# Performance work log

Measured on AMD Instinct MI355X. Metric: run time of the kernel, lower is better.

The kernel has to match this reference:

```python
import jax, jax.numpy as jnp
import numpy as np

EMB = 512
HEADS = 8
WINDOW = 128


def setup_inputs() -> dict:
    key = jax.random.key(0)
    ks = jax.random.split(key, 9)
    s = 1.0 / np.sqrt(EMB)
    x = jax.random.normal(ks[0], (2, 4096, EMB), dtype=jnp.float32)
    mk = lambda k: jax.random.uniform(k, (EMB, EMB), jnp.float32, -s, s)
    mb = lambda k: jax.random.uniform(k, (EMB,), jnp.float32, -s, s)
    return {
        "x": x,
        "Wq": mk(ks[1]), "bq": mb(ks[2]),
        "Wk": mk(ks[3]), "bk": mb(ks[4]),
        "Wv": mk(ks[5]), "bv": mb(ks[6]),
        "Wo": mk(ks[7]), "bo": mb(ks[8]),
    }


def _split_heads(y, b, n):
    # [b, n, emb] -> [b, h, n, d]
    return y.reshape(b, n, HEADS, EMB // HEADS).transpose(0, 2, 1, 3)


def reference(x, Wq, bq, Wk, bk, Wv, bv, Wo, bo):
    b, n, _ = x.shape
    q = _split_heads(x @ Wq.T + bq, b, n)
    k = _split_heads(x @ Wk.T + bk, b, n)
    v = _split_heads(x @ Wv.T + bv, b, n)
    energy = jnp.einsum('bhqd,bhkd->bhqk', q, k)  # [b,h,n,n]
    idx = jnp.arange(n)
    # banded mask: disallowed where |i - j| > window (matches torch loop)
    disallow = jnp.abs(idx[:, None] - idx[None, :]) > WINDOW
    fmin = jnp.float32(np.finfo(np.float32).min)
    energy = jnp.where(disallow[None, None], fmin, energy)
    att = jax.nn.softmax(energy / jnp.float32(np.sqrt(EMB)), axis=-1)
    out = jnp.einsum('bhql,bhld->bhqd', att, v)
    out = out.transpose(0, 2, 1, 3).reshape(b, n, EMB)
    return out @ Wo.T + bo
```

## Files before the change

kernel.cpp:

```cpp
#include <hip/hip_runtime.h>

#define EMB 512
#define HEADS 8
#define HD 64
#define NSEQ 4096
#define BATCH 2
#define WINDOW 128

typedef unsigned short u16;
typedef __attribute__((ext_vector_type(8))) short bf16x8;
typedef __attribute__((ext_vector_type(4))) float f32x4;

#define XS 4194304u
#define WS 262144u
#define BS 512u

__device__ __forceinline__ float bf2f(u16 u) {
    union { unsigned int i; float f; } x;
    x.i = ((unsigned int)u) << 16;
    return x.f;
}

__device__ __forceinline__ u16 f2bf(float f) {
    union { float f; unsigned int i; } x;
    x.f = f;
    unsigned int i = x.i;
    unsigned int lsb = (i >> 16) & 1u;
    i += 0x7fffu + lsb;
    return (u16)(i >> 16);
}

struct raw8 { uint4 lo, hi; };

__device__ __forceinline__ raw8 loadraw8(const void* base, size_t off, int isbf) {
    raw8 r;
    if (isbf) {
        r.lo = *(const uint4*)((const u16*)base + off);
    } else {
        const float* f = (const float*)base + off;
        r.lo = *(const uint4*)f;
        r.hi = *(const uint4*)(f + 4);
    }
    return r;
}

__device__ __forceinline__ uint4 cvt8(const raw8& r, int isbf) {
    if (isbf) return r.lo;
    const float* a = (const float*)&r.lo;
    const float* b = (const float*)&r.hi;
    uint4 o;
    o.x = (unsigned)f2bf(a[0]) | ((unsigned)f2bf(a[1]) << 16);
    o.y = (unsigned)f2bf(a[2]) | ((unsigned)f2bf(a[3]) << 16);
    o.z = (unsigned)f2bf(b[0]) | ((unsigned)f2bf(b[1]) << 16);
    o.w = (unsigned)f2bf(b[2]) | ((unsigned)f2bf(b[3]) << 16);
    return o;
}

__device__ __forceinline__ int probe_bf16(const void* p) {
    const int lane = threadIdx.x & 63;
    u16 w = ((const u16*)p)[lane * 2];
    int e = (w >> 7) & 0xff;
    bool sane = (w == 0) || (e >= 100 && e <= 140);
    unsigned long long m = __ballot(sane);
    return __popcll(m) >= 48;
}

__global__ __launch_bounds__(256)
void prepass(const void* __restrict__ x,
             const void* __restrict__ Wq, const void* __restrict__ bq,
             const void* __restrict__ Wk, const void* __restrict__ bk,
             const void* __restrict__ Wv, const void* __restrict__ bv,
             const void* __restrict__ Wo, const void* __restrict__ bo,
             u16* __restrict__ xb, u16* __restrict__ wb, u16* __restrict__ bb,
             int* __restrict__ flags)
{
    const int fx  = probe_bf16(x);
    const int fwq = probe_bf16(Wq), fbq = probe_bf16(bq);
    const int fwk = probe_bf16(Wk), fbk = probe_bf16(bk);
    const int fwv = probe_bf16(Wv), fbv = probe_bf16(bv);
    const int fwo = probe_bf16(Wo), fbo = probe_bf16(bo);
    if (blockIdx.x == 0 && threadIdx.x == 0) flags[0] = fx;

    size_t idx = ((size_t)blockIdx.x * 256 + threadIdx.x) * 8;
    const size_t T_X = XS, T_W = XS + 4 * (size_t)WS, T_ALL = T_W + 4 * (size_t)BS;
    if (idx >= T_ALL) return;

    const void* src; int fl; u16* dst; size_t off;
    if (idx < T_X) {
        src = x; fl = fx; dst = xb; off = idx;
    } else if (idx < T_W) {
        size_t w = idx - T_X;
        int wi = (int)(w / WS); off = w % WS;
        src = (wi == 0) ? Wq : (wi == 1) ? Wk : (wi == 2) ? Wv : Wo;
        fl  = (wi == 0) ? fwq : (wi == 1) ? fwk : (wi == 2) ? fwv : fwo;
        dst = wb + (size_t)wi * WS;
    } else {
        size_t b = idx - T_W;
        int bi = (int)(b / BS); off = b % BS;
        src = (bi == 0) ? bq : (bi == 1) ? bk : (bi == 2) ? bv : bo;
        fl  = (bi == 0) ? fbq : (bi == 1) ? fbk : (bi == 2) ? fbv : fbo;
        dst = bb + (size_t)bi * BS;
    }
    *(uint4*)(dst + off) = cvt8(loadraw8(src, off, fl), fl);
}

__global__ __launch_bounds__(512)
void qkv_gemm(const u16* __restrict__ X, const u16* __restrict__ Wall,
              const u16* __restrict__ ball,
              u16* __restrict__ qo, u16* __restrict__ ko, u16* __restrict__ vo)
{
    __shared__ __align__(16) u16 As2[2][128 * 32];
    __shared__ __align__(16) u16 Bs2[2][128 * 32];

    const int tid  = threadIdx.x;
    const int wave = tid >> 6;
    const int lane = tid & 63;
    const int quad = lane >> 4;
    const int l16  = lane & 15;
    const int wm = wave >> 2, wn = wave & 3;

    const int m0 = blockIdx.x * 128;
    const int by = blockIdx.y;
    const int wsel = by >> 2;
    const int n0 = (by & 3) * 128;

    const u16* W  = Wall + (size_t)wsel * WS;
    const u16* bi = ball + (size_t)wsel * BS;
    const float oscale = (wsel == 0) ? 0.04419417382415922f : 1.0f;

    const u16* PA = (wsel == 2) ? W : X;
    const u16* PB = (wsel == 2) ? X : W;
    const int abase = (wsel == 2) ? n0 : m0;
    const int bbase = (wsel == 2) ? m0 : n0;

    f32x4 acc[4][2];
#pragma unroll
    for (int i = 0; i < 4; ++i)
#pragma unroll
        for (int j = 0; j < 2; ++j)
            acc[i][j] = (f32x4){0.f, 0.f, 0.f, 0.f};

    const int r1 = tid >> 2, k1 = (tid & 3) * 8;

    const u16* pa = PA + (size_t)(abase + r1) * EMB + k1;
    const u16* pb = PB + (size_t)(bbase + r1) * EMB + k1;

    uint4 a1 = *(const uint4*)pa;
    uint4 b1 = *(const uint4*)pb;
    *(uint4*)&As2[0][tid * 8] = a1;
    *(uint4*)&Bs2[0][tid * 8] = b1;
    a1 = *(const uint4*)(pa + 32);
    b1 = *(const uint4*)(pb + 32);
    __syncthreads();

    for (int kt = 0; kt < 16; ++kt) {
        const int cur = kt & 1;

        bf16x8 af[4], bfr[2];
#pragma unroll
        for (int i = 0; i < 4; ++i)
            af[i] = *(const bf16x8*)&As2[cur][(wm * 64 + i * 16 + l16) * 32 + quad * 8];
#pragma unroll
        for (int j = 0; j < 2; ++j)
            bfr[j] = *(const bf16x8*)&Bs2[cur][(wn * 32 + j * 16 + l16) * 32 + quad * 8];

        if (kt < 15) {
            *(uint4*)&As2[cur ^ 1][tid * 8] = a1;
            *(uint4*)&Bs2[cur ^ 1][tid * 8] = b1;
        }
        if (kt < 14) {
            const int kk0 = (kt + 2) * 32;
            a1 = *(const uint4*)(pa + kk0);
            b1 = *(const uint4*)(pb + kk0);
        }

#pragma unroll
        for (int i = 0; i < 4; ++i)
#pragma unroll
            for (int j = 0; j < 2; ++j)
                acc[i][j] = __builtin_amdgcn_mfma_f32_16x16x32_bf16(af[i], bfr[j], acc[i][j], 0, 0, 0);

        if (kt < 15) __syncthreads();
    }

    if (wsel != 2) {
#pragma unroll
        for (int j = 0; j < 2; ++j) {
            const int col = n0 + wn * 32 + j * 16 + l16;
            const float bv_ = bf2f(bi[col]);
            const int h = col >> 6, d = col & 63;
            u16* out = (wsel == 0) ? qo : ko;
#pragma unroll
            for (int i = 0; i < 4; ++i) {
#pragma unroll
                for (int r = 0; r < 4; ++r) {
                    const int row = m0 + wm * 64 + i * 16 + quad * 4 + r;
                    const int b = row >> 12, n = row & 4095;
                    out[(((size_t)(b * HEADS + h) * NSEQ) + n) * HD + d] =
                        f2bf((acc[i][j][r] + bv_) * oscale);
                }
            }
        }
    } else {
#pragma unroll
        for (int i = 0; i < 4; ++i) {
#pragma unroll
            for (int r = 0; r < 4; ++r) {
                const int dglob = n0 + wm * 64 + i * 16 + quad * 4 + r;
                const float bv_ = bf2f(bi[dglob]);
                const int h = dglob >> 6, dd = dglob & 63;
#pragma unroll
                for (int j = 0; j < 2; ++j) {
                    const int ncol = m0 + wn * 32 + j * 16 + l16;
                    const int b = ncol >> 12, n = ncol & 4095;
                    vo[((size_t)(b * HEADS + h) * HD + dd) * NSEQ + n] =
                        f2bf(acc[i][j][r] + bv_);
                }
            }
        }
    }
}

#define KP 72
#define VP 72
__global__ __launch_bounds__(256)
void attn_mfma(const u16* __restrict__ q, const u16* __restrict__ k,
               const u16* __restrict__ vt, u16* __restrict__ ao)
{
    __shared__ __align__(16) u16 Ks2[2][64 * KP];
    __shared__ __align__(16) u16 Vt2[2][64 * VP];
    __shared__ __align__(16) u16 Vones[16 * VP];
    __shared__ __align__(16) u16 Pb[4][16 * KP];

    const int tid  = threadIdx.x;
    const int wave = tid >> 6;
    const int lane = tid & 63;
    const int quad = lane >> 4;
    const int l16  = lane & 15;

    int wg = blockIdx.y * 64 + blockIdx.x;
    wg = (wg & 7) * 128 + (wg >> 3);
    const int bh = wg >> 6;
    const int q0 = (wg & 63) * 64;

    const int qw = q0 + wave * 16;
    const size_t base = (size_t)bh * NSEQ * HD;
    const bool interior = (q0 >= 128) && (q0 <= NSEQ - 192);

    if (tid < VP) {
        Vones[tid] = (u16)0x3f80;
#pragma unroll
        for (int rr = 1; rr < 16; ++rr) Vones[rr * VP + tid] = 0;
    }

    bf16x8 qa0 = *(const bf16x8*)(q + base + (size_t)(qw + l16) * HD + quad * 8);
    bf16x8 qa1 = *(const bf16x8*)(q + base + (size_t)(qw + l16) * HD + 32 + quad * 8);

    f32x4 O[4], O4;
#pragma unroll
    for (int t = 0; t < 4; ++t) O[t] = (f32x4){0.f, 0.f, 0.f, 0.f};
    O4 = (f32x4){0.f, 0.f, 0.f, 0.f};

    const int key_s[2] = { tid >> 3, (tid + 256) >> 3 };
    const int ch8      = (tid & 7) * 8;

    const int pacol = (quad * 8) ^ ((l16 >> 2) << 4);

    uint4 pkv[2], pvv[2];
#pragma unroll
    for (int s = 0; s < 2; ++s) {
        int kg = q0 - 128 + key_s[s];
        kg = (kg < 0) ? 0 : (kg > NSEQ - 1 ? NSEQ - 1 : kg);
        pkv[s] = *(const uint4*)(k + base + (size_t)kg * HD + ch8);
        int kc = q0 - 128 + ch8;
        kc = (kc < 0) ? 0 : (kc > NSEQ - 8 ? NSEQ - 8 : kc);
        pvv[s] = *(const uint4*)(vt + base + (size_t)key_s[s] * NSEQ + kc);
    }
#pragma unroll
    for (int s = 0; s < 2; ++s) {
        *(uint4*)&Ks2[0][key_s[s] * KP + ch8] = pkv[s];
        *(uint4*)&Vt2[0][key_s[s] * VP + ch8] = pvv[s];
    }
#pragma unroll
    for (int s = 0; s < 2; ++s) {
        int kg = q0 - 64 + key_s[s];
        kg = (kg < 0) ? 0 : (kg > NSEQ - 1 ? NSEQ - 1 : kg);
        pkv[s] = *(const uint4*)(k + base + (size_t)kg * HD + ch8);
        int kc = q0 - 64 + ch8;
        kc = (kc < 0) ? 0 : (kc > NSEQ - 8 ? NSEQ - 8 : kc);
        pvv[s] = *(const uint4*)(vt + base + (size_t)key_s[s] * NSEQ + kc);
    }
    __syncthreads();

    for (int c = 0; c < 5; ++c) {
        const int cur = c & 1;
        const int kbase = q0 - 128 + c * 64;

        if (c < 4) {
#pragma unroll
            for (int s = 0; s < 2; ++s) {
                *(uint4*)&Ks2[cur ^ 1][key_s[s] * KP + ch8] = pkv[s];
                *(uint4*)&Vt2[cur ^ 1][key_s[s] * VP + ch8] = pvv[s];
            }
        }
        if (c < 3) {
            const int nb = kbase + 128;
#pragma unroll
            for (int s = 0; s < 2; ++s) {
                int kg = nb + key_s[s];
                kg = (kg < 0) ? 0 : (kg > NSEQ - 1 ? NSEQ - 1 : kg);
                pkv[s] = *(const uint4*)(k + base + (size_t)kg * HD + ch8);
                int kc = nb + ch8;
                kc = (kc < 0) ? 0 : (kc > NSEQ - 8 ? NSEQ - 8 : kc);
                pvv[s] = *(const uint4*)(vt + base + (size_t)key_s[s] * NSEQ + kc);
            }
        }

        const int gdk = kbase - qw;
        const bool act = (gdk <= 143) && (gdk >= -191) &&
                         (kbase > -64) && (kbase < NSEQ);
        if (act) {
            f32x4 sv[4];
#pragma unroll
            for (int t = 0; t < 4; ++t) {
                const int dk = gdk + t * 16;
                if (dk >= -143 && dk <= 143) {
                    bf16x8 b0 = *(const bf16x8*)&Ks2[cur][(t * 16 + l16) * KP + quad * 8];
                    bf16x8 b1 = *(const bf16x8*)&Ks2[cur][(t * 16 + l16) * KP + 32 + quad * 8];
                    f32x4 sacc = (f32x4){0.f, 0.f, 0.f, 0.f};
                    sacc = __builtin_amdgcn_mfma_f32_16x16x32_bf16(qa0, b0, sacc, 0, 0, 0);
                    sacc = __builtin_amdgcn_mfma_f32_16x16x32_bf16(qa1, b1, sacc, 0, 0, 0);
                    if (!interior || dk < -113 || dk > 113) {
                        const int jg = kbase + t * 16 + l16;
                        const bool jok = ((unsigned)jg) < (unsigned)NSEQ;
#pragma unroll
                        for (int r = 0; r < 4; ++r) {
                            const int iq = qw + quad * 4 + r;
                            const bool band = ((unsigned)(iq - jg + WINDOW)) <= (unsigned)(2 * WINDOW);
                            if (!(jok && band)) sacc[r] = -1e30f;
                        }
                    }
                    sv[t] = sacc;
                } else {
                    sv[t] = (f32x4){-1e30f, -1e30f, -1e30f, -1e30f};
                }
            }

#pragma unroll
            for (int t = 0; t < 4; ++t) {
                const int tc = (t ^ quad) * 16 + l16;
#pragma unroll
                for (int r = 0; r < 4; ++r) {
                    const float pv = __expf(fminf(sv[t][r], 40.f));
                    Pb[wave][(quad * 4 + r) * KP + tc] = f2bf(pv);
                }
            }

#pragma unroll
            for (int ks2 = 0; ks2 < 2; ++ks2) {
                bf16x8 pa = *(const bf16x8*)&Pb[wave][l16 * KP + (pacol ^ (ks2 * 32))];
#pragma unroll
                for (int t = 0; t < 4; ++t) {
                    bf16x8 vb = *(const bf16x8*)&Vt2[cur][(t * 16 + l16) * VP + ks2 * 32 + quad * 8];
                    O[t] = __builtin_amdgcn_mfma_f32_16x16x32_bf16(pa, vb, O[t], 0, 0, 0);
                }
                bf16x8 vb4 = *(const bf16x8*)&Vones[l16 * VP + ks2 * 32 + quad * 8];
                O4 = __builtin_amdgcn_mfma_f32_16x16x32_bf16(pa, vb4, O4, 0, 0, 0);
            }
        }

        if (c < 4) __syncthreads();
    }

    const int bb = bh >> 3, hh = bh & 7;
    float rl[4];
#pragma unroll
    for (int r = 0; r < 4; ++r) {
        const float ls = __shfl(O4[r], lane & 48, 64);
        rl[r] = 1.f / ls;
    }
#pragma unroll
    for (int t = 0; t < 4; ++t)
#pragma unroll
        for (int r = 0; r < 4; ++r) {
            const int iq = qw + quad * 4 + r;
            ao[((size_t)(bb * NSEQ + iq)) * EMB + hh * HD + t * 16 + l16] =
                f2bf(O[t][r] * rl[r]);
        }
}

__global__ __launch_bounds__(512)
void out_gemm(const u16* __restrict__ A, const u16* __restrict__ W,
              const u16* __restrict__ bias, void* __restrict__ out,
              const int* __restrict__ flags)
{
    __shared__ __align__(16) u16 As2[2][128 * 32];
    __shared__ __align__(16) u16 Bs2[2][128 * 32];

    const int tid  = threadIdx.x;
    const int wave = tid >> 6;
    const int lane = tid & 63;
    const int quad = lane >> 4;
    const int l16  = lane & 15;
    const int wm = wave >> 2, wn = wave & 3;

    const int m0 = blockIdx.x * 128;
    const int n0 = blockIdx.y * 128;
    const int fo = flags[0];

    f32x4 acc[4][2];
#pragma unroll
    for (int i = 0; i < 4; ++i)
#pragma unroll
        for (int j = 0; j < 2; ++j)
            acc[i][j] = (f32x4){0.f, 0.f, 0.f, 0.f};

    const int r1 = tid >> 2, k1 = (tid & 3) * 8;

    uint4 a1 = *(const uint4*)(A + (size_t)(m0 + r1) * EMB + k1);
    uint4 b1 = *(const uint4*)(W + (size_t)(n0 + r1) * EMB + k1);
    *(uint4*)&As2[0][tid * 8] = a1;
    *(uint4*)&Bs2[0][tid * 8] = b1;
    a1 = *(const uint4*)(A + (size_t)(m0 + r1) * EMB + 32 + k1);
    b1 = *(const uint4*)(W + (size_t)(n0 + r1) * EMB + 32 + k1);
    __syncthreads();

    for (int kt = 0; kt < 16; ++kt) {
        const int cur = kt & 1;

        bf16x8 af[4], bfr[2];
#pragma unroll
        for (int i = 0; i < 4; ++i)
            af[i] = *(const bf16x8*)&As2[cur][(wm * 64 + i * 16 + l16) * 32 + quad * 8];
#pragma unroll
        for (int j = 0; j < 2; ++j)
            bfr[j] = *(const bf16x8*)&Bs2[cur][(wn * 32 + j * 16 + l16) * 32 + quad * 8];

        if (kt < 15) {
            *(uint4*)&As2[cur ^ 1][tid * 8] = a1;
            *(uint4*)&Bs2[cur ^ 1][tid * 8] = b1;
        }
        if (kt < 14) {
            const int kk0 = (kt + 2) * 32;
            a1 = *(const uint4*)(A + (size_t)(m0 + r1) * EMB + kk0 + k1);
            b1 = *(const uint4*)(W + (size_t)(n0 + r1) * EMB + kk0 + k1);
        }

#pragma unroll
        for (int i = 0; i < 4; ++i)
#pragma unroll
            for (int j = 0; j < 2; ++j)
                acc[i][j] = __builtin_amdgcn_mfma_f32_16x16x32_bf16(af[i], bfr[j], acc[i][j], 0, 0, 0);

        if (kt < 15) __syncthreads();
    }

#pragma unroll
    for (int j = 0; j < 2; ++j) {
        const int col = n0 + wn * 32 + j * 16 + l16;
        const float bv_ = bf2f(bias[col]);
#pragma unroll
        for (int i = 0; i < 4; ++i) {
#pragma unroll
            for (int r = 0; r < 4; ++r) {
                const int row = m0 + wm * 64 + i * 16 + quad * 4 + r;
                const float val = acc[i][j][r] + bv_;
                const size_t idx = (size_t)row * EMB + col;
                if (fo) ((u16*)out)[idx] = f2bf(val);
                else    ((float*)out)[idx] = val;
            }
        }
    }
}

extern "C" void kernel_launch(void* const* d_in, const int* in_sizes, int n_in,
                              void* d_out, int out_size, void* d_ws, size_t ws_size,
                              hipStream_t stream)
{
    const size_t HSZ  = (size_t)BATCH * HEADS * NSEQ * HD;
    char* base = (char*)d_ws;
    int* flags = (int*)base;
    const size_t off = 256;

    u16* xb = (u16*)(base + off);
    u16* wb = xb + XS;
    u16* bb = wb + 4 * (size_t)WS;
    u16* kk = bb + 4 * (size_t)BS;
    u16* vv = kk + HSZ;
    u16* ao = vv + HSZ;
    u16* qq = ao + HSZ;

    const size_t need_t1 = off + 2 * (XS + 4 * (size_t)WS + 4 * (size_t)BS + 4 * HSZ);
    if (ws_size < need_t1) {
        qq = (u16*)d_out;
    }

    prepass<<<dim3(2561), 256, 0, stream>>>(d_in[0], d_in[1], d_in[2], d_in[3],
                                            d_in[4], d_in[5], d_in[6], d_in[7],
                                            d_in[8], xb, wb, bb, flags);
    qkv_gemm<<<dim3(64, 12), 512, 0, stream>>>(xb, wb, bb, qq, kk, vv);
    attn_mfma<<<dim3(64, 16), 256, 0, stream>>>(qq, kk, vv, ao);
    out_gemm<<<dim3(64, 4), 512, 0, stream>>>(ao, wb + 3 * (size_t)WS, bb + 3 * (size_t)BS,
                                              d_out, flags);
}
```

Measured before the change: 146.0 us.

## Probe only the source tensor in prepass; use 1024 threads in out_gemm

```diff
diff --git a/kernel.cpp b/kernel.cpp
--- a/kernel.cpp
+++ b/kernel.cpp
@@ -74,33 +74,26 @@
              u16* __restrict__ xb, u16* __restrict__ wb, u16* __restrict__ bb,
              int* __restrict__ flags)
 {
-    const int fx  = probe_bf16(x);
-    const int fwq = probe_bf16(Wq), fbq = probe_bf16(bq);
-    const int fwk = probe_bf16(Wk), fbk = probe_bf16(bk);
-    const int fwv = probe_bf16(Wv), fbv = probe_bf16(bv);
-    const int fwo = probe_bf16(Wo), fbo = probe_bf16(bo);
-    if (blockIdx.x == 0 && threadIdx.x == 0) flags[0] = fx;
-
     size_t idx = ((size_t)blockIdx.x * 256 + threadIdx.x) * 8;
     const size_t T_X = XS, T_W = XS + 4 * (size_t)WS, T_ALL = T_W + 4 * (size_t)BS;
     if (idx >= T_ALL) return;
 
-    const void* src; int fl; u16* dst; size_t off;
+    const void* src; u16* dst; size_t off;
     if (idx < T_X) {
-        src = x; fl = fx; dst = xb; off = idx;
+        src = x; dst = xb; off = idx;
     } else if (idx < T_W) {
         size_t w = idx - T_X;
         int wi = (int)(w / WS); off = w % WS;
         src = (wi == 0) ? Wq : (wi == 1) ? Wk : (wi == 2) ? Wv : Wo;
-        fl  = (wi == 0) ? fwq : (wi == 1) ? fwk : (wi == 2) ? fwv : fwo;
         dst = wb + (size_t)wi * WS;
     } else {
         size_t b = idx - T_W;
         int bi = (int)(b / BS); off = b % BS;
         src = (bi == 0) ? bq : (bi == 1) ? bk : (bi == 2) ? bv : bo;
-        fl  = (bi == 0) ? fbq : (bi == 1) ? fbk : (bi == 2) ? fbv : fbo;
         dst = bb + (size_t)bi * BS;
     }
+    const int fl = probe_bf16(src);
+    if (idx == 0) flags[0] = fl;
     *(uint4*)(dst + off) = cvt8(loadraw8(src, off, fl), fl);
 }
 
@@ -389,7 +382,7 @@
         }
 }
 
-__global__ __launch_bounds__(512)
+__global__ __launch_bounds__(1024)
 void out_gemm(const u16* __restrict__ A, const u16* __restrict__ W,
               const u16* __restrict__ bias, void* __restrict__ out,
               const int* __restrict__ flags)
@@ -408,46 +401,47 @@
     const int n0 = blockIdx.y * 128;
     const int fo = flags[0];
 
-    f32x4 acc[4][2];
-#pragma unroll
-    for (int i = 0; i < 4; ++i)
+    f32x4 acc[2][2];
+#pragma unroll
+    for (int i = 0; i < 2; ++i)
 #pragma unroll
         for (int j = 0; j < 2; ++j)
             acc[i][j] = (f32x4){0.f, 0.f, 0.f, 0.f};
 
-    const int r1 = tid >> 2, k1 = (tid & 3) * 8;
-
-    uint4 a1 = *(const uint4*)(A + (size_t)(m0 + r1) * EMB + k1);
-    uint4 b1 = *(const uint4*)(W + (size_t)(n0 + r1) * EMB + k1);
-    *(uint4*)&As2[0][tid * 8] = a1;
-    *(uint4*)&Bs2[0][tid * 8] = b1;
-    a1 = *(const uint4*)(A + (size_t)(m0 + r1) * EMB + 32 + k1);
-    b1 = *(const uint4*)(W + (size_t)(n0 + r1) * EMB + 32 + k1);
+    const int half = tid >> 9;
+    const int t2   = tid & 511;
+    const int r1 = t2 >> 2, k1 = (t2 & 3) * 8;
+
+    const u16* P = half ? (W + (size_t)(n0 + r1) * EMB + k1)
+                        : (A + (size_t)(m0 + r1) * EMB + k1);
+
+    uint4 v1 = *(const uint4*)P;
+    if (half) *(uint4*)&Bs2[0][t2 * 8] = v1;
+    else      *(uint4*)&As2[0][t2 * 8] = v1;
+    v1 = *(const uint4*)(P + 32);
     __syncthreads();
 
     for (int kt = 0; kt < 16; ++kt) {
         const int cur = kt & 1;
 
-        bf16x8 af[4], bfr[2];
-#pragma unroll
-        for (int i = 0; i < 4; ++i)
-            af[i] = *(const bf16x8*)&As2[cur][(wm * 64 + i * 16 + l16) * 32 + quad * 8];
+        bf16x8 af[2], bfr[2];
+#pragma unroll
+        for (int i = 0; i < 2; ++i)
+            af[i] = *(const bf16x8*)&As2[cur][(wm * 32 + i * 16 + l16) * 32 + quad * 8];
 #pragma unroll
         for (int j = 0; j < 2; ++j)
             bfr[j] = *(const bf16x8*)&Bs2[cur][(wn * 32 + j * 16 + l16) * 32 + quad * 8];
 
         if (kt < 15) {
-            *(uint4*)&As2[cur ^ 1][tid * 8] = a1;
-            *(uint4*)&Bs2[cur ^ 1][tid * 8] = b1;
+            if (half) *(uint4*)&Bs2[cur ^ 1][t2 * 8] = v1;
+            else      *(uint4*)&As2[cur ^ 1][t2 * 8] = v1;
         }
         if (kt < 14) {
-            const int kk0 = (kt + 2) * 32;
-            a1 = *(const uint4*)(A + (size_t)(m0 + r1) * EMB + kk0 + k1);
-            b1 = *(const uint4*)(W + (size_t)(n0 + r1) * EMB + kk0 + k1);
-        }
-
-#pragma unroll
-        for (int i = 0; i < 4; ++i)
+            v1 = *(const uint4*)(P + (kt + 2) * 32);
+        }
+
+#pragma unroll
+        for (int i = 0; i < 2; ++i)
 #pragma unroll
             for (int j = 0; j < 2; ++j)
                 acc[i][j] = __builtin_amdgcn_mfma_f32_16x16x32_bf16(af[i], bfr[j], acc[i][j], 0, 0, 0);
@@ -460,10 +454,10 @@
         const int col = n0 + wn * 32 + j * 16 + l16;
         const float bv_ = bf2f(bias[col]);
 #pragma unroll
-        for (int i = 0; i < 4; ++i) {
+        for (int i = 0; i < 2; ++i) {
 #pragma unroll
             for (int r = 0; r < 4; ++r) {
-                const int row = m0 + wm * 64 + i * 16 + quad * 4 + r;
+                const int row = m0 + wm * 32 + i * 16 + quad * 4 + r;
                 const float val = acc[i][j][r] + bv_;
                 const size_t idx = (size_t)row * EMB + col;
                 if (fo) ((u16*)out)[idx] = f2bf(val);
@@ -500,6 +494,6 @@
                                             d_in[8], xb, wb, bb, flags);
     qkv_gemm<<<dim3(64, 12), 512, 0, stream>>>(xb, wb, bb, qq, kk, vv);
     attn_mfma<<<dim3(64, 16), 256, 0, stream>>>(qq, kk, vv, ao);
-    out_gemm<<<dim3(64, 4), 512, 0, stream>>>(ao, wb + 3 * (size_t)WS, bb + 3 * (size_t)BS,
-                                              d_out, flags);
-}
+    out_gemm<<<dim3(64, 4), 1024, 0, stream>>>(ao, wb + 3 * (size_t)WS, bb + 3 * (size_t)BS,
+                                               d_out, flags);
+}
```

Result: no change. 146.0 us, median of 2 (+0.0%).
